# Performance work log

Hardware: AMD Instinct MI355X
Metric: run time of the kernel (lower is better)

## Reference

```python
import jax, jax.numpy as jnp
import numpy as np

C = 512          # channels
G = 32           # GroupNorm groups (flax default)
H = 8            # num_heads
EPS = 1e-6       # GroupNorm epsilon (flax default)
SPATIAL = (64, 64)


def setup_inputs() -> dict:
    key = jax.random.key(0)
    k1, k2 = jax.random.split(key)
    x = jax.random.normal(k1, SPATIAL + (C,), dtype=jnp.float32)
    gn_scale = jnp.ones((C,), dtype=jnp.float32)
    gn_bias = jnp.zeros((C,), dtype=jnp.float32)
    w_qkv = jax.random.normal(k2, (C, 3 * C), dtype=jnp.float32) / np.sqrt(C)
    b_qkv = jnp.zeros((3 * C,), dtype=jnp.float32)
    return {"x": x, "gn_scale": gn_scale, "gn_bias": gn_bias,
            "w_qkv": w_qkv, "b_qkv": b_qkv}


def reference(x, gn_scale, gn_bias, w_qkv, b_qkv):
    spatial_shape = x.shape[:-1]
    T = int(np.prod(spatial_shape))
    xf = x.reshape(T, C)

    # GroupNorm over (all spatial positions, channels within group) per group
    xg = xf.reshape(T, G, C // G)
    mean = jnp.mean(xg, axis=(0, 2), keepdims=True)
    var = jnp.var(xg, axis=(0, 2), keepdims=True)
    xn = ((xg - mean) * jax.lax.rsqrt(var + EPS)).reshape(T, C)
    xn = xn * gn_scale + gn_bias

    # QKV projection; note strided split: reshape (T, 3C) -> (T, C, 3)
    qkv = (xn @ w_qkv + b_qkv).reshape(T, C, 3)
    q, k, v = qkv[..., 0], qkv[..., 1], qkv[..., 2]

    ch = C // H
    scale = 1.0 / np.sqrt(np.sqrt(ch))
    qh = (q * scale).reshape(T, H, ch)
    kh = (k * scale).reshape(T, H, ch)
    vh = v.reshape(T, H, ch)

    w = jnp.einsum('thc,shc->ths', qh, kh)      # (T, H, T) attention scores
    w = jax.nn.softmax(w, axis=-1)
    a = jnp.einsum('ths,shc->thc', w, vh)       # (T, H, ch)
    return a.reshape(spatial_shape + (C,))
```

## Files before the change

### kernel.cpp

```cpp
#include <hip/hip_runtime.h>
#include <hip/hip_bf16.h>
#include <stdint.h>

typedef __attribute__((ext_vector_type(8))) short bf16x8;
typedef __attribute__((ext_vector_type(4))) float f32x4;
typedef __attribute__((ext_vector_type(16))) float f32x16;
typedef unsigned short u16;
typedef unsigned int u32;

constexpr int T  = 4096;
constexpr int C  = 512;
constexpr int H  = 8;
constexpr int CH = 64;
constexpr float EPS = 1e-6f;
constexpr float QKS   = 0.35355339059327378f;
constexpr float QKS_Q = 0.35355339059327378f * 1.4426950408889634f;

__device__ __forceinline__ float bf2f(u16 u) {
    union { unsigned int i; float f; } v; v.i = ((unsigned int)u) << 16; return v.f;
}
__device__ __forceinline__ u16 f2bf(float f) {
    union { float f; unsigned int i; } v; v.f = f;
    return (u16)((v.i + 0x7FFFu + ((v.i >> 16) & 1u)) >> 16);
}
__device__ __forceinline__ u32 pk2bf(float a, float b) {
    __hip_bfloat162 h = __float22bfloat162_rn(make_float2(a, b));
    u32 r; __builtin_memcpy(&r, &h, 4); return r;
}
__device__ __forceinline__ float ldin(const void* p, int i, int f32) {
    return f32 ? ((const float*)p)[i] : bf2f(((const u16*)p)[i]);
}
__device__ __forceinline__ void async16(const void* g, void* l) {
    __builtin_amdgcn_global_load_lds(
        (const __attribute__((address_space(1))) void*)g,
        (__attribute__((address_space(3))) void*)l,
        16, 0, 0);
}
__device__ __forceinline__ u32 pktrunc(float a, float b) {
    u32 ua = __float_as_uint(a), ub = __float_as_uint(b);
    return __builtin_amdgcn_perm(ub, ua, 0x07060302u);
}

__global__ void k_stats1(const void* x, float* gs2, int* flag) {
    int b = blockIdx.x, tid = threadIdx.x;
    int lane = tid & 63, w = tid >> 6;
    __shared__ int cnt;
    __shared__ float red[4][32][2];
    if (tid == 0) cnt = 0;
    __syncthreads();
    const u16* u = (const u16*)x;
    int huge = 0;
    for (int i = tid; i < 1024; i += 256) {
        float a = fabsf(bf2f(u[i]));
        if (!(a < 1e4f)) huge++;
    }
    if (huge) atomicAdd(&cnt, huge);
    __syncthreads();
    int f32 = (cnt >= 8) ? 1 : 0;
    if (b == 0 && tid == 0) *flag = f32;
    float s1 = 0.f, s2 = 0.f;
    if (f32) {
        const float4* xp = (const float4*)x + b * 4096;
        #pragma unroll
        for (int i = 0; i < 16; i++) {
            float4 v = xp[i * 256 + tid];
            s1 += (v.x + v.y) + (v.z + v.w);
            s2 += (v.x*v.x + v.y*v.y) + (v.z*v.z + v.w*v.w);
        }
        s1 += __shfl_xor(s1, 1); s2 += __shfl_xor(s2, 1);
        s1 += __shfl_xor(s1, 2); s2 += __shfl_xor(s2, 2);
        if ((lane & 3) == 0) {
            int gl = (lane >> 2) + 16 * (w & 1);
            red[w][gl][0] = s1; red[w][gl][1] = s2;
        }
        __syncthreads();
        if (tid < 32) {
            int g = tid, w0 = (g < 16) ? 0 : 1;
            gs2[b * 64 + g * 2]     = red[w0][g][0] + red[w0 + 2][g][0];
            gs2[b * 64 + g * 2 + 1] = red[w0][g][1] + red[w0 + 2][g][1];
        }
    } else {
        const uint4* xp = (const uint4*)x + b * 2048;
        #pragma unroll
        for (int i = 0; i < 8; i++) {
            uint4 v = xp[i * 256 + tid];
            float f[8] = { bf2f((u16)(v.x&0xffff)), bf2f((u16)(v.x>>16)),
                           bf2f((u16)(v.y&0xffff)), bf2f((u16)(v.y>>16)),
                           bf2f((u16)(v.z&0xffff)), bf2f((u16)(v.z>>16)),
                           bf2f((u16)(v.w&0xffff)), bf2f((u16)(v.w>>16)) };
            #pragma unroll
            for (int j = 0; j < 8; j++) { s1 += f[j]; s2 += f[j]*f[j]; }
        }
        s1 += __shfl_xor(s1, 1); s2 += __shfl_xor(s2, 1);
        if ((lane & 1) == 0) { red[w][lane >> 1][0] = s1; red[w][lane >> 1][1] = s2; }
        __syncthreads();
        if (tid < 32) {
            int g = tid;
            gs2[b * 64 + g * 2]     = red[0][g][0]+red[1][g][0]+red[2][g][0]+red[3][g][0];
            gs2[b * 64 + g * 2 + 1] = red[0][g][1]+red[1][g][1]+red[2][g][1]+red[3][g][1];
        }
    }
}

__global__ void k_fuse(const void* x, const float* __restrict__ gs2,
                       const void* gsc, const void* gbi, const void* wq,
                       u16* __restrict__ xn, u16* __restrict__ wt,
                       const int* __restrict__ flag) {
    int bx = blockIdx.x, tid = threadIdx.x;
    int f32 = *flag;
    if (bx < 1024) {
        __shared__ float sred[64];
        if (tid < 64) {
            float a0 = 0.f, a1 = 0.f, a2 = 0.f, a3 = 0.f;
            const float* p = gs2 + tid;
            #pragma unroll
            for (int b = 0; b < 32; b++) {
                a0 += p[(4*b + 0) * 64];
                a1 += p[(4*b + 1) * 64];
                a2 += p[(4*b + 2) * 64];
                a3 += p[(4*b + 3) * 64];
            }
            sred[tid] = (a0 + a1) + (a2 + a3);
        }
        __syncthreads();
        int idx = (bx * 256 + tid) * 8;
        int c = idx & (C - 1);
        int g = c >> 4;
        float mean = sred[2 * g] * (1.0f / 65536.0f);
        float var  = sred[2 * g + 1] * (1.0f / 65536.0f) - mean * mean;
        float rstd = rsqrtf(var + EPS);
        float v[8];
        if (f32) {
            float4 x0 = *(const float4*)((const float*)x + idx);
            float4 x1 = *(const float4*)((const float*)x + idx + 4);
            v[0]=x0.x; v[1]=x0.y; v[2]=x0.z; v[3]=x0.w;
            v[4]=x1.x; v[5]=x1.y; v[6]=x1.z; v[7]=x1.w;
        } else {
            uint4 u = *(const uint4*)((const u16*)x + idx);
            v[0]=bf2f((u16)(u.x&0xffff)); v[1]=bf2f((u16)(u.x>>16));
            v[2]=bf2f((u16)(u.y&0xffff)); v[3]=bf2f((u16)(u.y>>16));
            v[4]=bf2f((u16)(u.z&0xffff)); v[5]=bf2f((u16)(u.z>>16));
            v[6]=bf2f((u16)(u.w&0xffff)); v[7]=bf2f((u16)(u.w>>16));
        }
        float r[8];
        #pragma unroll
        for (int i = 0; i < 8; i++) {
            float a = rstd * ldin(gsc, c + i, f32);
            r[i] = v[i] * a + (ldin(gbi, c + i, f32) - mean * a);
        }
        uint4 o;
        o.x = pk2bf(r[0], r[1]); o.y = pk2bf(r[2], r[3]);
        o.z = pk2bf(r[4], r[5]); o.w = pk2bf(r[6], r[7]);
        *(uint4*)(xn + idx) = o;
    } else {
        __shared__ u16 Wl[48][64];
        int b = bx - 1024;
        int k0 = (b >> 5) * 64, c0 = (b & 31) * 48;
        #pragma unroll
        for (int it = 0; it < 3; it++) {
            int u_ = it * 256 + tid;
            int r = u_ / 12, cu = u_ % 12;
            int gi = (k0 + r) * 1536 + c0 + cu * 4;
            float v0, v1, v2, v3;
            if (f32) {
                float4 t4 = *(const float4*)((const float*)wq + gi);
                v0 = t4.x; v1 = t4.y; v2 = t4.z; v3 = t4.w;
            } else {
                uint2 t2 = *(const uint2*)((const u16*)wq + gi);
                v0 = bf2f((u16)(t2.x & 0xffff)); v1 = bf2f((u16)(t2.x >> 16));
                v2 = bf2f((u16)(t2.y & 0xffff)); v3 = bf2f((u16)(t2.y >> 16));
            }
            Wl[cu*4+0][r] = f2bf(v0); Wl[cu*4+1][r] = f2bf(v1);
            Wl[cu*4+2][r] = f2bf(v2); Wl[cu*4+3][r] = f2bf(v3);
        }
        __syncthreads();
        #pragma unroll
        for (int it = 0; it < 2; it++) {
            int u_ = it * 256 + tid;
            if (u_ < 384) {
                int mrow = u_ >> 3, kc = u_ & 7;
                int j = mrow >> 4, cci = mrow & 15;
                int m = j * 512 + (c0 / 3) + cci;
                int cl = 3 * cci + j;
                uint4 val = *(const uint4*)&Wl[cl][kc * 8];
                *(uint4*)(wt + m * 512 + k0 + kc * 8) = val;
            }
        }
    }
}

__global__ __launch_bounds__(256) void k_gemm(
    const u16* __restrict__ xn, const u16* __restrict__ wt,
    const void* __restrict__ bq, const int* __restrict__ flag,
    u16* __restrict__ qh, u16* __restrict__ kh, u16* __restrict__ vt)
{
    __shared__ char smem[49152];
    u16* Al = (u16*)smem;
    u16* Bl = (u16*)(smem + 16384);
    int bx = blockIdx.x;
    int bm = bx & 63, bn = bx >> 6;
    int tid = threadIdx.x;
    int w = tid >> 6, lane = tid & 63, quad = lane >> 4, l15 = lane & 15;
    f32x4 acc[4][2] = {};
    const u16* Ag = xn + bm * 64 * 512;
    const u16* Bg = wt + bn * 128 * 512;

    #pragma unroll
    for (int i = 0; i < 2; i++) {
        int L = i * 256 + tid, row = L >> 3, cc = ((L & 7) ^ (row & 7)) * 8;
        async16(Ag + row * 512 + cc, (void*)(Al + L * 8));
    }
    #pragma unroll
    for (int i = 0; i < 4; i++) {
        int L = i * 256 + tid, row = L >> 3, cc = ((L & 7) ^ (row & 7)) * 8;
        async16(Bg + row * 512 + cc, (void*)(Bl + L * 8));
    }

    #pragma unroll
    for (int ki = 0; ki < 8; ki++) {
        __syncthreads();
        if (ki < 7) {
            int kn = (ki + 1) * 64;
            int bo = ((ki + 1) & 1);
            #pragma unroll
            for (int i = 0; i < 2; i++) {
                int L = i * 256 + tid, row = L >> 3, cc = ((L & 7) ^ (row & 7)) * 8;
                async16(Ag + row * 512 + kn + cc, (void*)(Al + bo * 4096 + L * 8));
            }
            #pragma unroll
            for (int i = 0; i < 4; i++) {
                int L = i * 256 + tid, row = L >> 3, cc = ((L & 7) ^ (row & 7)) * 8;
                async16(Bg + row * 512 + kn + cc, (void*)(Bl + bo * 8192 + L * 8));
            }
        }
        const u16* Ab = Al + (ki & 1) * 4096;
        const u16* Bb = Bl + (ki & 1) * 8192;
        #pragma unroll
        for (int kk = 0; kk < 2; kk++) {
            bf16x8 af[4], bfr[2];
            #pragma unroll
            for (int mi = 0; mi < 4; mi++) {
                int row = mi * 16 + l15;
                af[mi] = *(const bf16x8*)(Ab + row * 64 + (((kk * 4 + quad) ^ (row & 7)) * 8));
            }
            #pragma unroll
            for (int ni = 0; ni < 2; ni++) {
                int row = w * 32 + ni * 16 + l15;
                bfr[ni] = *(const bf16x8*)(Bb + row * 64 + (((kk * 4 + quad) ^ (row & 7)) * 8));
            }
            #pragma unroll
            for (int mi = 0; mi < 4; mi++)
                #pragma unroll
                for (int ni = 0; ni < 2; ni++)
                    acc[mi][ni] = __builtin_amdgcn_mfma_f32_16x16x32_bf16(
                        af[mi], bfr[ni], acc[mi][ni], 0, 0, 0);
        }
    }
    int f32 = *flag;
    int t_base = bm * 64;
    int j = bn >> 2;
    if (j < 2) {
        u16* dst = j ? kh : qh;
        float s = j ? QKS : QKS_Q;
        #pragma unroll
        for (int ni = 0; ni < 2; ni++) {
            int n = bn * 128 + w * 32 + ni * 16 + l15;
            int r = n & 511, hh = r >> 6, cc = r & 63;
            float bias = ldin(bq, 3 * r + j, f32);
            #pragma unroll
            for (int mi = 0; mi < 4; mi++) {
                int tq = t_base + mi * 16 + quad * 4;
                #pragma unroll
                for (int rg = 0; rg < 4; rg++)
                    dst[(hh * T + tq + rg) * CH + cc] = f2bf((acc[mi][ni][rg] + bias) * s);
            }
        }
    } else {
        __syncthreads();
        u16* Tt = (u16*)smem;
        u16* Tw = Tt + w * 2048;
        int rbase = (bn - 8) * 128 + w * 32;
        int hh = rbase >> 6;
        #pragma unroll
        for (int ni = 0; ni < 2; ni++) {
            int r = rbase + ni * 16 + l15;
            float bias = ldin(bq, 3 * (r & 511) + 2, f32);
            int rl = ni * 16 + l15;
            #pragma unroll
            for (int mi = 0; mi < 4; mi++) {
                uint2 pv;
                pv.x = pk2bf(acc[mi][ni][0] + bias, acc[mi][ni][1] + bias);
                pv.y = pk2bf(acc[mi][ni][2] + bias, acc[mi][ni][3] + bias);
                int cs = (mi * 2 + (quad >> 1)) ^ (rl & 7);
                *(uint2*)((u32*)Tw + rl * 32 + cs * 4 + (quad & 1) * 2) = pv;
            }
        }
        int cc_hi = (w & 1) * 32;
        #pragma unroll
        for (int rr = 0; rr < 4; rr++) {
            int rl = rr * 8 + (lane >> 3);
            int g = lane & 7;
            int cA = (g & ~1) ^ (rl & 7);
            int cB = ((g & ~1) + 1) ^ (rl & 7);
            int ofs = (g & 1) * 4;
            uint2 a = *(const uint2*)(Tw + rl * 64 + cA * 8 + ofs);
            uint2 b = *(const uint2*)(Tw + rl * 64 + cB * 8 + ofs);
            *(uint4*)(vt + (hh * CH + cc_hi + rl) * T + t_base + g * 8) =
                make_uint4(a.x, a.y, b.x, b.y);
        }
    }
}

__global__ __launch_bounds__(256, 4) void k_attn(
    const u16* __restrict__ qh, const u16* __restrict__ kh,
    const u16* __restrict__ vt, float* __restrict__ opart, float* __restrict__ ls)
{
    __shared__ char lds[32768];
    u16* K0 = (u16*)lds;
    u16* V0 = (u16*)(lds + 16384);
    int bx = blockIdx.x;
    int h = bx >> 7, qb = (bx >> 2) & 31, ks = bx & 3;
    int t0 = qb * 128;
    int tid = threadIdx.x;
    int w = tid >> 6, lane = tid & 63;
    int l31 = lane & 31, hi = lane >> 5;

    const u16* Kg = kh + (h * T + ks * 1024) * CH;
    const u16* Vg = vt + h * CH * T + ks * 1024;

    int L0 = tid,       r0 = L0 >> 3, c0 = ((L0 & 7) ^ (r0 & 7)) * 8;
    int L1 = 256 + tid, r1 = L1 >> 3, c1 = ((L1 & 7) ^ (r1 & 7)) * 8;
    const u16* kp0 = Kg + r0 * CH + c0;
    const u16* kp1 = Kg + r1 * CH + c1;
    const u16* vp0 = Vg + r0 * T + c0;
    const u16* vp1 = Vg + r1 * T + c1;

    int off[2][4];
    #pragma unroll
    for (int rt = 0; rt < 2; rt++)
        #pragma unroll
        for (int c = 0; c < 4; c++) {
            int row = rt * 32 + l31;
            off[rt][c] = row * 64 + (((2 * c + hi) ^ (row & 7)) * 8);
        }

    bf16x8 bq[4];
    {
        const u16* qrow = qh + (h * T + t0 + w * 32 + l31) * CH;
        #pragma unroll
        for (int ksi = 0; ksi < 4; ksi++)
            bq[ksi] = *(const bf16x8*)(qrow + ksi * 16 + hi * 8);
    }

    async16(kp0, (void*)(K0 + L0 * 8));
    async16(kp1, (void*)(K0 + L1 * 8));
    async16(vp0, (void*)(V0 + L0 * 8));
    async16(vp1, (void*)(V0 + L1 * 8));

    f32x16 o[2] = {};
    float lsum = 0.f;

    for (int kt = 0; kt < 16; kt++) {
        int par = (kt & 1) * 4096;
        const u16* Kc = K0 + par;
        const u16* Vc = V0 + par;
        __syncthreads();
        if (kt < 15) {
            int nx = ((kt + 1) & 1) * 4096;
            int ko = (kt + 1) * 64 * CH;
            int vo = (kt + 1) * 64;
            async16(kp0 + ko, (void*)(K0 + nx + L0 * 8));
            async16(kp1 + ko, (void*)(K0 + nx + L1 * 8));
            async16(vp0 + vo, (void*)(V0 + nx + L0 * 8));
            async16(vp1 + vo, (void*)(V0 + nx + L1 * 8));
        }
        f32x16 sa[2] = {};
        #pragma unroll
        for (int t = 0; t < 2; t++)
            #pragma unroll
            for (int ksi = 0; ksi < 4; ksi++) {
                bf16x8 aK = *(const bf16x8*)(Kc + off[t][ksi]);
                sa[t] = __builtin_amdgcn_mfma_f32_32x32x16_bf16(aK, bq[ksi], sa[t], 0, 0, 0);
            }
        u32 bp[4][4];
        #pragma unroll
        for (int t = 0; t < 2; t++) {
            float rs = 0.f;
            #pragma unroll
            for (int pi = 0; pi < 8; pi++) {
                float e0 = exp2f(sa[t][2 * pi]);
                float e1 = exp2f(sa[t][2 * pi + 1]);
                rs += e0 + e1;
                bp[2 * t + (pi >> 2)][pi & 3] = pktrunc(e0, e1);
            }
            lsum += rs;
        }
        #pragma unroll
        for (int dt = 0; dt < 2; dt++)
            #pragma unroll
            for (int kst = 0; kst < 4; kst++) {
                bf16x8 aV = *(const bf16x8*)(Vc + off[dt][kst]);
                bf16x8 bpv;
                __builtin_memcpy(&bpv, bp[kst], 16);
                o[dt] = __builtin_amdgcn_mfma_f32_32x32x16_bf16(aV, bpv, o[dt], 0, 0, 0);
            }
    }
    lsum += __shfl_xor(lsum, 32);

    __syncthreads();
    float* Sw = (float*)(lds + w * 6144);
    int qg = t0 + w * 32;
    int q2 = lane >> 1, half = lane & 1;
    #pragma unroll
    for (int dt = 0; dt < 2; dt++) {
        #pragma unroll
        for (int reg = 0; reg < 16; reg++) {
            int dl = (reg & 3) + 8 * (reg >> 2) + 4 * hi;
            Sw[l31 * 33 + dl] = o[dt][reg];
        }
        const float* src = Sw + q2 * 33 + half * 16;
        float* dst = opart + ((ks * 8 + h) * T + qg + q2) * 64 + dt * 32 + half * 16;
        #pragma unroll
        for (int i = 0; i < 4; i++)
            *(f32x4*)(dst + i * 4) = *(const f32x4*)(src + i * 4);
    }
    if (hi == 0) ls[(ks * 8 + h) * T + qg + l31] = lsum;
}

__global__ void k_fin(const float* __restrict__ opart, const float* __restrict__ ls,
                      void* __restrict__ out, const int* __restrict__ flag) {
    int idx = (blockIdx.x * 256 + threadIdx.x) * 8;
    int d0 = idx & 63;
    int ht = idx >> 6;
    int t = ht & (T - 1), h = ht >> 12;
    float inv = 1.0f / (ls[ht] + ls[32768 + ht] + ls[65536 + ht] + ls[98304 + ht]);
    float v[8] = {};
    #pragma unroll
    for (int ks = 0; ks < 4; ks++) {
        float4 a0 = *(const float4*)(opart + ks * 2097152 + idx);
        float4 a1 = *(const float4*)(opart + ks * 2097152 + idx + 4);
        v[0] += a0.x; v[1] += a0.y; v[2] += a0.z; v[3] += a0.w;
        v[4] += a1.x; v[5] += a1.y; v[6] += a1.z; v[7] += a1.w;
    }
    #pragma unroll
    for (int i = 0; i < 8; i++) v[i] *= inv;
    int gbase = t * C + h * CH + d0;
    if (*flag) {
        *(float4*)((float*)out + gbase)     = make_float4(v[0], v[1], v[2], v[3]);
        *(float4*)((float*)out + gbase + 4) = make_float4(v[4], v[5], v[6], v[7]);
    } else {
        uint4 o;
        o.x = pk2bf(v[0], v[1]); o.y = pk2bf(v[2], v[3]);
        o.z = pk2bf(v[4], v[5]); o.w = pk2bf(v[6], v[7]);
        *(uint4*)((u16*)out + gbase) = o;
    }
}

extern "C" void kernel_launch(void* const* d_in, const int* in_sizes, int n_in,
                              void* d_out, int out_size, void* d_ws, size_t ws_size,
                              hipStream_t stream) {
    const void* x   = d_in[0];
    const void* gsc = d_in[1];
    const void* gbi = d_in[2];
    const void* wq  = d_in[3];
    const void* bq  = d_in[4];
    char* ws = (char*)d_ws;
    int*   flag = (int*)ws;
    char* base = ws + 8192;
    u16* qh = (u16*)(base);
    u16* kh = (u16*)(base + 4194304);
    u16* vt = (u16*)(base + 8388608);
    u16* xn = (u16*)(base + 12582912);
    u16* wt = (u16*)(base + 16777216);
    float* opart = (float*)(base + 12582912);
    float* ls    = (float*)(base + 46137344);
    float* gs2   = (float*)(base + 46661632);

    hipLaunchKernelGGL(k_stats1, dim3(128),  dim3(256), 0, stream, x, gs2, flag);
    hipLaunchKernelGGL(k_fuse,   dim3(1280), dim3(256), 0, stream, x, gs2, gsc, gbi, wq, xn, wt, flag);
    hipLaunchKernelGGL(k_gemm,   dim3(768),  dim3(256), 0, stream, xn, wt, bq, flag, qh, kh, vt);
    hipLaunchKernelGGL(k_attn,   dim3(1024), dim3(256), 0, stream, qh, kh, vt, opart, ls);
    hipLaunchKernelGGL(k_fin,    dim3(1024), dim3(256), 0, stream, opart, ls, d_out, flag);
}
```

Measured before the change: 160.1 us.

## Split attention keys eight ways and store partial outputs in bf16

Splits the key dimension of the attention kernel into 8 chunks of 512 keys instead of 4 chunks of 1024, doubling the grid to 2048 blocks for better occupancy across CUs. The partial outputs are stored as bf16 instead of fp32, so the extra partials do not double the traffic in the reduction step. The finish kernel sums 8 partials and their row sums. Each block now has a shorter loop, so prologue and epilogue costs are paid more often, and rounding the partials to bf16 adds precision loss.

After: 157.2 us. About the same (-1.8%).

```diff
diff --git a/kernel.cpp b/kernel.cpp
--- a/kernel.cpp
+++ b/kernel.cpp
@@ -313,20 +313,20 @@
 
 __global__ __launch_bounds__(256, 4) void k_attn(
     const u16* __restrict__ qh, const u16* __restrict__ kh,
-    const u16* __restrict__ vt, float* __restrict__ opart, float* __restrict__ ls)
+    const u16* __restrict__ vt, u16* __restrict__ opart, float* __restrict__ ls)
 {
     __shared__ char lds[32768];
     u16* K0 = (u16*)lds;
     u16* V0 = (u16*)(lds + 16384);
     int bx = blockIdx.x;
-    int h = bx >> 7, qb = (bx >> 2) & 31, ks = bx & 3;
+    int h = bx >> 8, qb = (bx >> 3) & 31, ks = bx & 7;
     int t0 = qb * 128;
     int tid = threadIdx.x;
     int w = tid >> 6, lane = tid & 63;
     int l31 = lane & 31, hi = lane >> 5;
 
-    const u16* Kg = kh + (h * T + ks * 1024) * CH;
-    const u16* Vg = vt + h * CH * T + ks * 1024;
+    const u16* Kg = kh + (h * T + ks * 512) * CH;
+    const u16* Vg = vt + h * CH * T + ks * 512;
 
     int L0 = tid,       r0 = L0 >> 3, c0 = ((L0 & 7) ^ (r0 & 7)) * 8;
     int L1 = 256 + tid, r1 = L1 >> 3, c1 = ((L1 & 7) ^ (r1 & 7)) * 8;
@@ -360,12 +360,12 @@
     f32x16 o[2] = {};
     float lsum = 0.f;
 
-    for (int kt = 0; kt < 16; kt++) {
+    for (int kt = 0; kt < 8; kt++) {
         int par = (kt & 1) * 4096;
         const u16* Kc = K0 + par;
         const u16* Vc = V0 + par;
         __syncthreads();
-        if (kt < 15) {
+        if (kt < 7) {
             int nx = ((kt + 1) & 1) * 4096;
             int ko = (kt + 1) * 64 * CH;
             int vo = (kt + 1) * 64;
@@ -419,28 +419,34 @@
             Sw[l31 * 33 + dl] = o[dt][reg];
         }
         const float* src = Sw + q2 * 33 + half * 16;
-        float* dst = opart + ((ks * 8 + h) * T + qg + q2) * 64 + dt * 32 + half * 16;
-        #pragma unroll
-        for (int i = 0; i < 4; i++)
-            *(f32x4*)(dst + i * 4) = *(const f32x4*)(src + i * 4);
+        u16* dst = opart + (size_t)((ks * 8 + h) * T + qg + q2) * 64 + dt * 32 + half * 16;
+        u32 pk[8];
+        #pragma unroll
+        for (int i = 0; i < 8; i++) pk[i] = pk2bf(src[2 * i], src[2 * i + 1]);
+        *(uint4*)(dst)     = make_uint4(pk[0], pk[1], pk[2], pk[3]);
+        *(uint4*)(dst + 8) = make_uint4(pk[4], pk[5], pk[6], pk[7]);
     }
     if (hi == 0) ls[(ks * 8 + h) * T + qg + l31] = lsum;
 }
 
-__global__ void k_fin(const float* __restrict__ opart, const float* __restrict__ ls,
+__global__ void k_fin(const u16* __restrict__ opart, const float* __restrict__ ls,
                       void* __restrict__ out, const int* __restrict__ flag) {
     int idx = (blockIdx.x * 256 + threadIdx.x) * 8;
     int d0 = idx & 63;
     int ht = idx >> 6;
     int t = ht & (T - 1), h = ht >> 12;
-    float inv = 1.0f / (ls[ht] + ls[32768 + ht] + ls[65536 + ht] + ls[98304 + ht]);
+    float lt = 0.f;
+    #pragma unroll
+    for (int s = 0; s < 8; s++) lt += ls[s * 32768 + ht];
+    float inv = 1.0f / lt;
     float v[8] = {};
     #pragma unroll
-    for (int ks = 0; ks < 4; ks++) {
-        float4 a0 = *(const float4*)(opart + ks * 2097152 + idx);
-        float4 a1 = *(const float4*)(opart + ks * 2097152 + idx + 4);
-        v[0] += a0.x; v[1] += a0.y; v[2] += a0.z; v[3] += a0.w;
-        v[4] += a1.x; v[5] += a1.y; v[6] += a1.z; v[7] += a1.w;
+    for (int s = 0; s < 8; s++) {
+        uint4 a = *(const uint4*)(opart + s * 2097152 + idx);
+        v[0] += bf2f((u16)(a.x & 0xffff)); v[1] += bf2f((u16)(a.x >> 16));
+        v[2] += bf2f((u16)(a.y & 0xffff)); v[3] += bf2f((u16)(a.y >> 16));
+        v[4] += bf2f((u16)(a.z & 0xffff)); v[5] += bf2f((u16)(a.z >> 16));
+        v[6] += bf2f((u16)(a.w & 0xffff)); v[7] += bf2f((u16)(a.w >> 16));
     }
     #pragma unroll
     for (int i = 0; i < 8; i++) v[i] *= inv;
@@ -472,13 +478,13 @@
     u16* vt = (u16*)(base + 8388608);
     u16* xn = (u16*)(base + 12582912);
     u16* wt = (u16*)(base + 16777216);
-    float* opart = (float*)(base + 12582912);
+    u16* opart = (u16*)(base + 12582912);
     float* ls    = (float*)(base + 46137344);
-    float* gs2   = (float*)(base + 46661632);
+    float* gs2   = (float*)(base + 47185920);
 
     hipLaunchKernelGGL(k_stats1, dim3(128),  dim3(256), 0, stream, x, gs2, flag);
     hipLaunchKernelGGL(k_fuse,   dim3(1280), dim3(256), 0, stream, x, gs2, gsc, gbi, wq, xn, wt, flag);
     hipLaunchKernelGGL(k_gemm,   dim3(768),  dim3(256), 0, stream, xn, wt, bq, flag, qh, kh, vt);
-    hipLaunchKernelGGL(k_attn,   dim3(1024), dim3(256), 0, stream, qh, kh, vt, opart, ls);
+    hipLaunchKernelGGL(k_attn,   dim3(2048), dim3(256), 0, stream, qh, kh, vt, opart, ls);
     hipLaunchKernelGGL(k_fin,    dim3(1024), dim3(256), 0, stream, opart, ls, d_out, flag);
 }
```
